# Kernel tuning notes

Hardware: AMD Instinct MI355X
Metric: run time of the kernel (lower is better)

Reference implementation:

```python
import jax, jax.numpy as jnp
import numpy as np

N, E = 50000, 800000
IN, HID, H, OUT = 128, 32, 4, 40
K_SAMPLE, EPS_K = 25.0, 1e-3  # fixed k=25 (no dp_budget), compute_beta eps


def _glorot(key, shape):
    fan_in, fan_out = shape[0], shape[-1]
    lim = jnp.sqrt(6.0 / (fan_in + fan_out))
    return jax.random.uniform(key, shape, jnp.float32, -lim, lim)


def setup_inputs() -> dict:
    key = jax.random.key(0)
    ks = jax.random.split(key, 16)
    x = jax.random.normal(ks[0], (N, IN), jnp.float32)
    edge_index = jax.random.randint(ks[1], (2, E), 0, N, jnp.int64)
    # layer 0: IN -> (H, HID)
    W0 = _glorot(ks[2], (IN, H * HID)); as0 = _glorot(ks[3], (H, HID)); ad0 = _glorot(ks[4], (H, HID)); b0 = jnp.zeros((H * HID,), jnp.float32)
    # layer 1: H*HID -> (H, HID)
    W1 = _glorot(ks[5], (H * HID, H * HID)); as1 = _glorot(ks[6], (H, HID)); ad1 = _glorot(ks[7], (H, HID)); b1 = jnp.zeros((H * HID,), jnp.float32)
    # layer 2: H*HID -> (1, OUT)
    W2 = _glorot(ks[8], (H * HID, OUT)); as2 = _glorot(ks[9], (1, OUT)); ad2 = _glorot(ks[10], (1, OUT)); b2 = jnp.zeros((OUT,), jnp.float32)
    # BatchNorm affine params (batch-stat mode, deterministic)
    g_bn0 = jnp.ones((H * HID,), jnp.float32); be_bn0 = jnp.zeros((H * HID,), jnp.float32)
    g_bn1 = jnp.ones((H * HID,), jnp.float32); be_bn1 = jnp.zeros((H * HID,), jnp.float32)
    return {"x": x, "edge_index": edge_index,
            "W0": W0, "as0": as0, "ad0": ad0, "b0": b0,
            "W1": W1, "as1": as1, "ad1": ad1, "b1": b1,
            "W2": W2, "as2": as2, "ad2": ad2, "b2": b2,
            "g_bn0": g_bn0, "be_bn0": be_bn0, "g_bn1": g_bn1, "be_bn1": be_bn1}


def gat_conv(x, src, dst, W, a_src, a_dst, bias, heads, d_out):
    # PyG GATConv, add_self_loops=False, concat over heads
    h = (x @ W).reshape(-1, heads, d_out)                       # [N,H,D]
    al_s = jnp.sum(h * a_src, axis=-1)                          # [N,H]
    al_d = jnp.sum(h * a_dst, axis=-1)                          # [N,H]
    e = jax.nn.leaky_relu(al_s[src] + al_d[dst], 0.2)           # [E,H]
    m = jax.ops.segment_max(e, dst, num_segments=N)
    m = jnp.where(jnp.isfinite(m), m, 0.0)                      # guard empty segments
    p = jnp.exp(e - m[dst])
    s = jax.ops.segment_sum(p, dst, num_segments=N)
    alpha = p / (s[dst] + 1e-16)                                # segment softmax over incoming edges
    out = jax.ops.segment_sum(alpha[:, :, None] * h[src], dst, num_segments=N)  # [N,H,D]
    return out.reshape(-1, heads * d_out) + bias


def batch_norm(x, gamma, beta):
    mu = jnp.mean(x, axis=0)
    var = jnp.mean(jnp.square(x - mu), axis=0)
    return gamma * (x - mu) * jax.lax.rsqrt(var + 1e-5) + beta


def beta_scale(l):
    return 1.0 + 1.0 / (l + 1.0) * (1.0 / (K_SAMPLE + EPS_K))


def reference(x, edge_index, W0, as0, ad0, b0, W1, as1, ad1, b1, W2, as2, ad2, b2,
              g_bn0, be_bn0, g_bn1, be_bn1):
    src, dst = edge_index[0], edge_index[1]
    h = gat_conv(x, src, dst, W0, as0, ad0, b0, H, HID)
    h = jax.nn.elu(batch_norm(h, g_bn0, be_bn0)) * beta_scale(0)
    h = gat_conv(h, src, dst, W1, as1, ad1, b1, H, HID)
    h = jax.nn.elu(batch_norm(h, g_bn1, be_bn1)) * beta_scale(1)
    h = gat_conv(h, src, dst, W2, as2, ad2, b2, 1, OUT)
    return jax.nn.log_softmax(h, axis=1)
```

## Files before the change

### kernel.cpp

```cpp
#include <hip/hip_runtime.h>
#include <math.h>

#define N_NODES 50000
#define N_EDGES 800000
#define DIN 128
#define DHID 128
#define NH 4
#define HID 32
#define DOUT 40

#define PB 128
#define NPB 391

typedef __fp16 fp16x2 __attribute__((ext_vector_type(2)));

static __device__ __forceinline__ float lrelu(float x) { return x > 0.f ? x : 0.2f * x; }

static __device__ __forceinline__ unsigned int pkh(float a, float b) {
    union { fp16x2 h2; unsigned int u; } cv;
    cv.h2 = __builtin_amdgcn_cvt_pkrtz(a, b);
    return cv.u;
}
static __device__ __forceinline__ unsigned short f2h(float a) {
    union { _Float16 h; unsigned short s; } cv;
    cv.h = (_Float16)a;
    return cv.s;
}

static __device__ __forceinline__ void fma8(float* acc, uint4 w, float p) {
    union { unsigned int u; _Float16 h[2]; } c0, c1, c2, c3;
    c0.u = w.x; c1.u = w.y; c2.u = w.z; c3.u = w.w;
    acc[0] = fmaf((float)c0.h[0], p, acc[0]);
    acc[1] = fmaf((float)c0.h[1], p, acc[1]);
    acc[2] = fmaf((float)c1.h[0], p, acc[2]);
    acc[3] = fmaf((float)c1.h[1], p, acc[3]);
    acc[4] = fmaf((float)c2.h[0], p, acc[4]);
    acc[5] = fmaf((float)c2.h[1], p, acc[5]);
    acc[6] = fmaf((float)c3.h[0], p, acc[6]);
    acc[7] = fmaf((float)c3.h[1], p, acc[7]);
}

static __device__ __forceinline__ float4 bnelu4(float4 x, float4 sc, float4 sh, float bs) {
    float y0 = fmaf(x.x, sc.x, sh.x);
    float y1 = fmaf(x.y, sc.y, sh.y);
    float y2 = fmaf(x.z, sc.z, sh.z);
    float y3 = fmaf(x.w, sc.w, sh.w);
    y0 = (y0 > 0.f ? y0 : __expf(y0) - 1.f) * bs;
    y1 = (y1 > 0.f ? y1 : __expf(y1) - 1.f) * bs;
    y2 = (y2 > 0.f ? y2 : __expf(y2) - 1.f) * bs;
    y3 = (y3 > 0.f ? y3 : __expf(y3) - 1.f) * bs;
    return {y0, y1, y2, y3};
}

__global__ __launch_bounds__(256) void bucket_hist_kernel(const int* __restrict__ dstv, int* __restrict__ bhist) {
    __shared__ int h[PB];
    if (threadIdx.x < PB) h[threadIdx.x] = 0;
    __syncthreads();
    for (int i = blockIdx.x * blockDim.x + threadIdx.x; i < N_EDGES; i += gridDim.x * blockDim.x)
        atomicAdd(&h[(unsigned)dstv[i] / NPB], 1);
    __syncthreads();
    if (threadIdx.x < PB) atomicAdd(&bhist[threadIdx.x], h[threadIdx.x]);
}

__global__ __launch_bounds__(128) void bucket_scan_kernel(const int* __restrict__ bhist,
                                                          int* __restrict__ bucket_base, int* __restrict__ cursor) {
    __shared__ int sA[PB], sB[PB];
    int t = threadIdx.x;
    sA[t] = bhist[t];
    __syncthreads();
    int* s = sA; int* d2 = sB;
    for (int off = 1; off < PB; off <<= 1) {
        d2[t] = s[t] + (t >= off ? s[t - off] : 0);
        __syncthreads();
        int* tmp = s; s = d2; d2 = tmp;
    }
    int excl = s[t] - bhist[t];
    bucket_base[t] = excl;
    cursor[t] = excl;
    if (t == PB - 1) bucket_base[PB] = s[t];
}

__global__ __launch_bounds__(256) void partition_kernel(const int* __restrict__ srcv, const int* __restrict__ dstv,
                                                        int* __restrict__ cursor, unsigned* __restrict__ part) {
    __shared__ unsigned rec[2048];
    __shared__ int cnt[PB], lofs[PB], gbase[PB];
    __shared__ int sA[PB], sB[PB];
    __shared__ int tot_s;
    const int t = threadIdx.x;
    const int base0 = blockIdx.x * 4096;
    for (int round = 0; round < 2; ++round) {
        int rbase = base0 + round * 2048;
        if (t < PB) cnt[t] = 0;
        __syncthreads();
        int myb[8]; int myr[8]; unsigned myrec[8];
#pragma unroll
        for (int i = 0; i < 8; ++i) {
            int e = rbase + i * 256 + t;
            bool valid = e < N_EDGES;
            int sv = valid ? srcv[e] : 0;
            int dv = valid ? dstv[e] : 0;
            myrec[i] = ((unsigned)sv << 16) | (unsigned)dv;
            int b = (unsigned)dv / NPB;
            myb[i] = valid ? b : -1;
            myr[i] = valid ? atomicAdd(&cnt[b], 1) : 0;
        }
        __syncthreads();
        if (t < PB) sA[t] = cnt[t];
        __syncthreads();
        int* s = sA; int* d2 = sB;
        for (int off = 1; off < PB; off <<= 1) {
            if (t < PB) d2[t] = s[t] + (t >= off ? s[t - off] : 0);
            __syncthreads();
            int* tmp = s; s = d2; d2 = tmp;
        }
        if (t < PB) {
            int c = cnt[t];
            lofs[t] = s[t] - c;
            gbase[t] = c > 0 ? atomicAdd(&cursor[t], c) : 0;
            if (t == PB - 1) tot_s = s[t];
        }
        __syncthreads();
#pragma unroll
        for (int i = 0; i < 8; ++i)
            if (myb[i] >= 0) rec[lofs[myb[i]] + myr[i]] = myrec[i];
        __syncthreads();
        int tot = tot_s;
#pragma unroll
        for (int i = 0; i < 8; ++i) {
            int lp = i * 256 + t;
            if (lp < tot) {
                unsigned r = rec[lp];
                int b = (r & 0xFFFFu) / NPB;
                part[gbase[b] + (lp - lofs[b])] = r;
            }
        }
        __syncthreads();
    }
}

__global__ __launch_bounds__(256) void bucket_csr_kernel(const unsigned* __restrict__ part, const int* __restrict__ bucket_base,
                                                         int* __restrict__ row_ptr, int* __restrict__ csr_src) {
    __shared__ int hist[512], sA[512], sB[512], cur[NPB];
    const int b = blockIdx.x, t = threadIdx.x;
    const int base = bucket_base[b];
    const int n = bucket_base[b + 1] - base;
    hist[t] = 0; hist[t + 256] = 0;
    __syncthreads();
    for (int i = t; i < n; i += 256)
        atomicAdd(&hist[(part[base + i] & 0xFFFFu) - b * NPB], 1);
    __syncthreads();
    sA[t] = hist[t]; sA[t + 256] = hist[t + 256];
    __syncthreads();
    int* s = sA; int* d2 = sB;
    for (int off = 1; off < 512; off <<= 1) {
        d2[t] = s[t] + (t >= off ? s[t - off] : 0);
        int u = t + 256;
        d2[u] = s[u] + (u >= off ? s[u - off] : 0);
        __syncthreads();
        int* tmp = s; s = d2; d2 = tmp;
    }
    for (int j = t; j < NPB; j += 256) {
        int node = b * NPB + j;
        int excl = s[j] - hist[j];
        if (node < N_NODES) row_ptr[node] = base + excl;
        cur[j] = excl;
    }
    if (b == PB - 1 && t == 0) row_ptr[N_NODES] = N_EDGES;
    __syncthreads();
    for (int i = t; i < n; i += 256) {
        unsigned r = part[base + i];
        int loc = (int)(r & 0xFFFFu) - b * NPB;
        int p = atomicAdd(&cur[loc], 1);
        csr_src[base + p] = (int)(r >> 16);
    }
}

__global__ __launch_bounds__(256) void gemm128_kernel(
    const float* __restrict__ X, const float* __restrict__ W,
    const float* __restrict__ a_src, const float* __restrict__ a_dst,
    const float* __restrict__ sums, const float* __restrict__ sqs,
    const float* __restrict__ gamma, const float* __restrict__ beta, float bscale, int apply_bn,
    unsigned int* __restrict__ Hout, float* __restrict__ als, float* __restrict__ ald) {
    __shared__ float Xs[32][68];
    __shared__ float Ws[32][64];
    __shared__ float scale_s[DHID], shift_s[DHID];
    const int t = threadIdx.x;
    const int tx = t & 15, ty = t >> 4;
    const int r0 = (blockIdx.x >> 1) * 64;
    const int c0 = (blockIdx.x & 1) * 64;
    const int sr = t >> 2, sa = t & 3;
    const int wk = t >> 4, wc = (t & 15) * 4;

    if (apply_bn && t < DHID) {
        float mu = sums[t] * (1.f / N_NODES);
        float var = sqs[t] * (1.f / N_NODES) - mu * mu;
        float sc = gamma[t] * rsqrtf(var + 1e-5f);
        scale_s[t] = sc;
        shift_s[t] = beta[t] - mu * sc;
    }
    __syncthreads();

    int gr = r0 + sr; gr = gr < N_NODES ? gr : N_NODES - 1;
    const float* Xrow = X + (size_t)gr * 128;
    float4 xpreA = *(const float4*)(Xrow + 8 * sa);
    float4 xpreB = *(const float4*)(Xrow + 8 * sa + 4);
    if (apply_bn) {
        xpreA = bnelu4(xpreA, *(const float4*)(scale_s + 8 * sa), *(const float4*)(shift_s + 8 * sa), bscale);
        xpreB = bnelu4(xpreB, *(const float4*)(scale_s + 8 * sa + 4), *(const float4*)(shift_s + 8 * sa + 4), bscale);
    }
    float4 wpreA = *(const float4*)(W + (size_t)wk * 128 + c0 + wc);
    float4 wpreB = *(const float4*)(W + (size_t)(wk + 16) * 128 + c0 + wc);

    float acc[4][4];
#pragma unroll
    for (int i = 0; i < 4; ++i)
#pragma unroll
        for (int c = 0; c < 4; ++c) acc[i][c] = 0.f;

    for (int step = 0; step < 4; ++step) {
        __syncthreads();
        Xs[8 * sa + 0][sr] = xpreA.x;
        Xs[8 * sa + 1][sr] = xpreA.y;
        Xs[8 * sa + 2][sr] = xpreA.z;
        Xs[8 * sa + 3][sr] = xpreA.w;
        Xs[8 * sa + 4][sr] = xpreB.x;
        Xs[8 * sa + 5][sr] = xpreB.y;
        Xs[8 * sa + 6][sr] = xpreB.z;
        Xs[8 * sa + 7][sr] = xpreB.w;
        *(float4*)&Ws[wk][wc] = wpreA;
        *(float4*)&Ws[wk + 16][wc] = wpreB;
        if (step < 3) {
            int k0 = (step + 1) * 32;
            xpreA = *(const float4*)(Xrow + k0 + 8 * sa);
            xpreB = *(const float4*)(Xrow + k0 + 8 * sa + 4);
            if (apply_bn) {
                xpreA = bnelu4(xpreA, *(const float4*)(scale_s + k0 + 8 * sa), *(const float4*)(shift_s + k0 + 8 * sa), bscale);
                xpreB = bnelu4(xpreB, *(const float4*)(scale_s + k0 + 8 * sa + 4), *(const float4*)(shift_s + k0 + 8 * sa + 4), bscale);
            }
            wpreA = *(const float4*)(W + (size_t)(k0 + wk) * 128 + c0 + wc);
            wpreB = *(const float4*)(W + (size_t)(k0 + wk + 16) * 128 + c0 + wc);
        }
        __syncthreads();
#pragma unroll
        for (int kk = 0; kk < 32; ++kk) {
            float4 xv = *(const float4*)&Xs[kk][4 * ty];
            float4 wv = *(const float4*)&Ws[kk][4 * tx];
            float xr[4] = {xv.x, xv.y, xv.z, xv.w};
            float wr[4] = {wv.x, wv.y, wv.z, wv.w};
#pragma unroll
            for (int i = 0; i < 4; ++i)
#pragma unroll
                for (int c = 0; c < 4; ++c)
                    acc[i][c] = fmaf(xr[i], wr[c], acc[i][c]);
        }
    }
    const int head = (c0 >> 5) + (tx >> 3);
    float asv[4], adv[4];
#pragma unroll
    for (int c = 0; c < 4; ++c) {
        asv[c] = a_src[(head & 1) * 32 + (4 * tx + c) % 32 + (head >> 1) * 64];
        adv[c] = a_dst[(head & 1) * 32 + (4 * tx + c) % 32 + (head >> 1) * 64];
    }
#pragma unroll
    for (int i = 0; i < 4; ++i) {
        int r = r0 + 4 * ty + i;
        bool valid = r < N_NODES;
        if (valid) {
            uint2 pk = {pkh(acc[i][0], acc[i][1]), pkh(acc[i][2], acc[i][3])};
            *(uint2*)(Hout + (size_t)r * 64 + (c0 >> 1) + 2 * tx) = pk;
        }
        float ps = 0.f, pd = 0.f;
#pragma unroll
        for (int c = 0; c < 4; ++c) {
            ps = fmaf(acc[i][c], asv[c], ps);
            pd = fmaf(acc[i][c], adv[c], pd);
        }
#pragma unroll
        for (int off = 1; off < 8; off <<= 1) {
            ps += __shfl_xor(ps, off);
            pd += __shfl_xor(pd, off);
        }
        if (valid && (tx & 7) == 0) {
            als[r * 4 + head] = ps;
            ald[r * 4 + head] = pd;
        }
    }
}

__global__ __launch_bounds__(256) void gemm40_kernel(
    const float* __restrict__ X, const float* __restrict__ W,
    const float* __restrict__ a_src, const float* __restrict__ a_dst,
    const float* __restrict__ sums, const float* __restrict__ sqs,
    const float* __restrict__ gamma, const float* __restrict__ beta, float bscale,
    unsigned short* __restrict__ Hout, float* __restrict__ als, float* __restrict__ ald) {
    __shared__ float Xs[64][36];
    __shared__ float Ws[40][36];
    __shared__ float scale_s[DHID], shift_s[DHID];
    const int t = threadIdx.x;
    const int tx = t & 7, ty = t >> 3;
    const int r0 = blockIdx.x * 64;
    const int sr = t >> 2, sa = t & 3;

    if (t < DHID) {
        float mu = sums[t] * (1.f / N_NODES);
        float var = sqs[t] * (1.f / N_NODES) - mu * mu;
        float sc = gamma[t] * rsqrtf(var + 1e-5f);
        scale_s[t] = sc;
        shift_s[t] = beta[t] - mu * sc;
    }
    __syncthreads();

    int gr = r0 + sr; gr = gr < N_NODES ? gr : N_NODES - 1;
    const float* Xrow = X + (size_t)gr * 128;
    float4 xpreA = bnelu4(*(const float4*)(Xrow + 8 * sa),
                          *(const float4*)(scale_s + 8 * sa), *(const float4*)(shift_s + 8 * sa), bscale);
    float4 xpreB = bnelu4(*(const float4*)(Xrow + 8 * sa + 4),
                          *(const float4*)(scale_s + 8 * sa + 4), *(const float4*)(shift_s + 8 * sa + 4), bscale);
    float wpre[5];
#pragma unroll
    for (int i = 0; i < 5; ++i) wpre[i] = W[t + 256 * i];

    float acc[2][5];
#pragma unroll
    for (int i = 0; i < 2; ++i)
#pragma unroll
        for (int j = 0; j < 5; ++j) acc[i][j] = 0.f;

    for (int step = 0; step < 4; ++step) {
        __syncthreads();
        *(float4*)&Xs[sr][8 * sa] = xpreA;
        *(float4*)&Xs[sr][8 * sa + 4] = xpreB;
#pragma unroll
        for (int i = 0; i < 5; ++i) {
            int idx = t + 256 * i;
            Ws[idx % 40][idx / 40] = wpre[i];
        }
        if (step < 3) {
            int k0 = (step + 1) * 32;
            xpreA = bnelu4(*(const float4*)(Xrow + k0 + 8 * sa),
                           *(const float4*)(scale_s + k0 + 8 * sa), *(const float4*)(shift_s + k0 + 8 * sa), bscale);
            xpreB = bnelu4(*(const float4*)(Xrow + k0 + 8 * sa + 4),
                           *(const float4*)(scale_s + k0 + 8 * sa + 4), *(const float4*)(shift_s + k0 + 8 * sa + 4), bscale);
#pragma unroll
            for (int i = 0; i < 5; ++i) wpre[i] = W[k0 * 40 + t + 256 * i];
        }
        __syncthreads();
#pragma unroll
        for (int kk4 = 0; kk4 < 8; ++kk4) {
            float4 xa = *(const float4*)&Xs[2 * ty][4 * kk4];
            float4 xb = *(const float4*)&Xs[2 * ty + 1][4 * kk4];
#pragma unroll
            for (int j = 0; j < 5; ++j) {
                float4 wv = *(const float4*)&Ws[tx + 8 * j][4 * kk4];
                acc[0][j] = fmaf(xa.x, wv.x, acc[0][j]);
                acc[0][j] = fmaf(xa.y, wv.y, acc[0][j]);
                acc[0][j] = fmaf(xa.z, wv.z, acc[0][j]);
                acc[0][j] = fmaf(xa.w, wv.w, acc[0][j]);
                acc[1][j] = fmaf(xb.x, wv.x, acc[1][j]);
                acc[1][j] = fmaf(xb.y, wv.y, acc[1][j]);
                acc[1][j] = fmaf(xb.z, wv.z, acc[1][j]);
                acc[1][j] = fmaf(xb.w, wv.w, acc[1][j]);
            }
        }
    }
    float asv[5], adv[5];
#pragma unroll
    for (int j = 0; j < 5; ++j) {
        asv[j] = a_src[tx + 8 * j];
        adv[j] = a_dst[tx + 8 * j];
    }
#pragma unroll
    for (int i = 0; i < 2; ++i) {
        int r = r0 + 2 * ty + i;
        bool valid = r < N_NODES;
        if (valid) {
#pragma unroll
            for (int j = 0; j < 5; ++j)
                Hout[(size_t)r * 40 + tx + 8 * j] = f2h(acc[i][j]);
        }
        float ps = 0.f, pd = 0.f;
#pragma unroll
        for (int j = 0; j < 5; ++j) {
            ps = fmaf(acc[i][j], asv[j], ps);
            pd = fmaf(acc[i][j], adv[j], pd);
        }
#pragma unroll
        for (int off = 1; off < 8; off <<= 1) {
            ps += __shfl_xor(ps, off);
            pd += __shfl_xor(pd, off);
        }
        if (valid && tx == 0) {
            als[r] = ps;
            ald[r] = pd;
        }
    }
}

__global__ __launch_bounds__(256) void agg128_kernel(
    const int* __restrict__ row_ptr, const int* __restrict__ csr_src,
    const unsigned int* __restrict__ Ht, const float* __restrict__ als, const float* __restrict__ ald,
    const float* __restrict__ bias, float* __restrict__ out) {
    __shared__ float s_p[4][256];
    __shared__ int s_u[4][64];
    int v = (blockIdx.x * blockDim.x + threadIdx.x) >> 6;
    v = __builtin_amdgcn_readfirstlane(v);
    int lane = threadIdx.x & 63;
    int wslot = threadIdx.x >> 6;
    if (v >= N_NODES) return;
    int beg = row_ptr[v], end = row_ptr[v + 1];
    float4 ad4 = *(const float4*)(ald + (size_t)v * 4);
    const int g = lane >> 4;
    const int li = lane & 15;
    const int hh = li >> 2;
    float tsum = 0.f;
    float acc[8];
#pragma unroll
    for (int j = 0; j < 8; ++j) acc[j] = 0.f;

    for (int cbeg = beg; cbeg < end; cbeg += 64) {
        int cnt = min(64, end - cbeg);
        bool act = lane < cnt;
        int u = act ? csr_src[cbeg + lane] : 0;
        float p0, p1, p2, p3;
        if (act) {
            float4 s4 = *(const float4*)(als + (size_t)u * 4);
            p0 = __expf(lrelu(s4.x + ad4.x));
            p1 = __expf(lrelu(s4.y + ad4.y));
            p2 = __expf(lrelu(s4.z + ad4.z));
            p3 = __expf(lrelu(s4.w + ad4.w));
        } else {
            p0 = p1 = p2 = p3 = 0.f;
        }
        s_u[wslot][lane] = u;
        float4 pv = {p0, p1, p2, p3};
        *(float4*)&s_p[wslot][lane * 4] = pv;
        for (int i = 0; i < cnt; i += 8) {
            int ea = i + g;
            int eb = i + 4 + g;
            int ua = s_u[wslot][ea];
            int ub = s_u[wslot][eb];
            float pa = s_p[wslot][ea * 4 + hh];
            float pb = s_p[wslot][eb * 4 + hh];
            uint4 wa = *(const uint4*)(Ht + (size_t)ua * 64 + li * 4);
            uint4 wb = *(const uint4*)(Ht + (size_t)ub * 64 + li * 4);
            tsum += pa + pb;
            fma8(acc, wa, pa);
            fma8(acc, wb, pb);
        }
    }
#pragma unroll
    for (int j = 0; j < 8; ++j) {
        acc[j] += __shfl_xor(acc[j], 16);
        acc[j] += __shfl_xor(acc[j], 32);
    }
    tsum += __shfl_xor(tsum, 16);
    tsum += __shfl_xor(tsum, 32);
    float inv = 1.f / (tsum + 1e-16f);
    if (g == 0) {
        float4 b0 = *(const float4*)(bias + 8 * li);
        float4 b1 = *(const float4*)(bias + 8 * li + 4);
        float4 o0 = {acc[0] * inv + b0.x, acc[1] * inv + b0.y, acc[2] * inv + b0.z, acc[3] * inv + b0.w};
        float4 o1 = {acc[4] * inv + b1.x, acc[5] * inv + b1.y, acc[6] * inv + b1.z, acc[7] * inv + b1.w};
        *(float4*)(out + (size_t)v * DHID + 8 * li) = o0;
        *(float4*)(out + (size_t)v * DHID + 8 * li + 4) = o1;
    }
}

__global__ __launch_bounds__(256) void agg40_kernel(
    const int* __restrict__ row_ptr, const int* __restrict__ csr_src,
    const uint4* __restrict__ Ht4, const float* __restrict__ als, const float* __restrict__ ald,
    const float* __restrict__ bias, float* __restrict__ out) {
    __shared__ float s_p[4][76];
    __shared__ int s_u[4][76];
    __shared__ float s_red[4][12][41];
    int v = (blockIdx.x * blockDim.x + threadIdx.x) >> 6;
    v = __builtin_amdgcn_readfirstlane(v);
    int lane = threadIdx.x & 63;
    int wslot = threadIdx.x >> 6;
    if (v >= N_NODES) return;
    int beg = row_ptr[v], end = row_ptr[v + 1];
    float adv = ald[v];
    const int g = lane / 5;
    const int li = lane - g * 5;
    const bool gact = lane < 60;
    if (lane < 12) { s_u[wslot][64 + lane] = 0; s_p[wslot][64 + lane] = 0.f; }
    float tsum = 0.f;
    float a[8];
#pragma unroll
    for (int j = 0; j < 8; ++j) a[j] = 0.f;

    for (int cbeg = beg; cbeg < end; cbeg += 64) {
        int cnt = min(64, end - cbeg);
        bool act = lane < cnt;
        int u = act ? csr_src[cbeg + lane] : 0;
        float p = act ? __expf(lrelu(als[u] + adv)) : 0.f;
        s_u[wslot][lane] = u;
        s_p[wslot][lane] = p;
        for (int i = 0; i < cnt; i += 12) {
            int e = i + g;
            int uu = s_u[wslot][e];
            float pp = s_p[wslot][e];
            uint4 w = {0u, 0u, 0u, 0u};
            if (gact) w = Ht4[(size_t)uu * 5 + li];
            if (gact) tsum += pp;
            fma8(a, w, pp);
        }
    }
    if (gact) {
#pragma unroll
        for (int j = 0; j < 8; ++j) s_red[wslot][g][li * 8 + j] = a[j];
        if (li == 0) s_red[wslot][g][40] = tsum;
    }
    bool fown = lane < DOUT;
    float accf = 0.f, T = 0.f;
#pragma unroll
    for (int g2 = 0; g2 < 12; ++g2) {
        if (fown) accf += s_red[wslot][g2][lane];
        T += s_red[wslot][g2][40];
    }
    float inv = 1.f / (T + 1e-16f);
    float z = fown ? (accf * inv + bias[lane]) : -1e30f;
    float zm = z;
#pragma unroll
    for (int off = 1; off < 64; off <<= 1) zm = fmaxf(zm, __shfl_xor(zm, off));
    float se = fown ? __expf(z - zm) : 0.f;
#pragma unroll
    for (int off = 1; off < 64; off <<= 1) se += __shfl_xor(se, off);
    float ls = zm + logf(se);
    if (fown) out[(size_t)v * DOUT + lane] = z - ls;
}

__global__ __launch_bounds__(256) void bn_stats_kernel(const float* __restrict__ X,
                                                       float* __restrict__ sums, float* __restrict__ sqs) {
    const int t = threadIdx.x;
    const int tid = blockIdx.x * 256 + t;
    const float4* X4 = (const float4*)X;
    float4 s = {0.f, 0.f, 0.f, 0.f}, q = {0.f, 0.f, 0.f, 0.f};
    for (int i = tid; i < N_NODES * 32; i += 500 * 256) {
        float4 vv = X4[i];
        s.x += vv.x; s.y += vv.y; s.z += vv.z; s.w += vv.w;
        q.x += vv.x * vv.x; q.y += vv.y * vv.y; q.z += vv.z * vv.z; q.w += vv.w * vv.w;
    }
    __shared__ float ls[1024], lq[1024];
    *(float4*)&ls[t * 4] = s;
    *(float4*)&lq[t * 4] = q;
    __syncthreads();
    if (t < 128) {
        int c4 = t >> 2, j = t & 3;
        float S = 0.f, Q = 0.f;
#pragma unroll
        for (int k = 0; k < 8; ++k) {
            S += ls[(c4 + 32 * k) * 4 + j];
            Q += lq[(c4 + 32 * k) * 4 + j];
        }
        atomicAdd(&sums[t], S);
        atomicAdd(&sqs[t], Q);
    }
}

extern "C" void kernel_launch(void* const* d_in, const int* in_sizes, int n_in,
                              void* d_out, int out_size, void* d_ws, size_t ws_size,
                              hipStream_t stream) {
    (void)in_sizes; (void)n_in; (void)out_size; (void)ws_size;
    const float* x = (const float*)d_in[0];
    const int* ei = (const int*)d_in[1];
    const float* W0 = (const float*)d_in[2];
    const float* as0 = (const float*)d_in[3];
    const float* ad0 = (const float*)d_in[4];
    const float* b0 = (const float*)d_in[5];
    const float* W1 = (const float*)d_in[6];
    const float* as1 = (const float*)d_in[7];
    const float* ad1 = (const float*)d_in[8];
    const float* b1 = (const float*)d_in[9];
    const float* W2 = (const float*)d_in[10];
    const float* as2 = (const float*)d_in[11];
    const float* ad2 = (const float*)d_in[12];
    const float* b2 = (const float*)d_in[13];
    const float* g_bn0 = (const float*)d_in[14];
    const float* be_bn0 = (const float*)d_in[15];
    const float* g_bn1 = (const float*)d_in[16];
    const float* be_bn1 = (const float*)d_in[17];
    float* out = (float*)d_out;

    const int* srcv = ei;
    const int* dstv = ei + N_EDGES;

    char* p = (char*)d_ws;
    auto carve = [&](size_t bytes) {
        char* q = p;
        p += (bytes + 255) & ~(size_t)255;
        return q;
    };
    unsigned int* h_bf = (unsigned int*)carve((size_t)N_NODES * 64 * 4);
    float* agg   = (float*)carve((size_t)N_NODES * DHID * 4);
    float* als   = (float*)carve((size_t)N_NODES * NH * 4);
    float* ald   = (float*)carve((size_t)N_NODES * NH * 4);
    int* row_ptr = (int*)carve((size_t)(N_NODES + 1) * 4);
    int* csr_src = (int*)carve((size_t)N_EDGES * 4);
    unsigned* part = (unsigned*)carve((size_t)N_EDGES * 4);
    int* bhist   = (int*)carve((PB + 512) * 4);
    float* sums0 = (float*)(bhist + PB);
    float* sqs0  = sums0 + 128;
    float* sums1 = sqs0 + 128;
    float* sqs1  = sums1 + 128;
    int* bucket_base = (int*)carve((PB + 1) * 4);
    int* cursor  = (int*)carve(PB * 4);

    const float bs0 = 1.0f + 1.0f / 25.001f;
    const float bs1 = 1.0f + 0.5f / 25.001f;

    const int RT64 = (N_NODES + 63) / 64;
    const int G128B = RT64 * 2;
    const int G40B = RT64;
    const int AB = (N_NODES * 64 + 255) / 256;
    const int PARTB = (N_EDGES + 4095) / 4096;

    hipMemsetAsync(bhist, 0, (PB + 512) * 4, stream);
    bucket_hist_kernel<<<400, 256, 0, stream>>>(dstv, bhist);
    bucket_scan_kernel<<<1, PB, 0, stream>>>(bhist, bucket_base, cursor);
    partition_kernel<<<PARTB, 256, 0, stream>>>(srcv, dstv, cursor, part);
    bucket_csr_kernel<<<PB, 256, 0, stream>>>(part, bucket_base, row_ptr, csr_src);

    gemm128_kernel<<<G128B, 256, 0, stream>>>(x, W0, as0, ad0, nullptr, nullptr, nullptr, nullptr, 1.f, 0, h_bf, als, ald);
    agg128_kernel<<<AB, 256, 0, stream>>>(row_ptr, csr_src, h_bf, als, ald, b0, agg);
    bn_stats_kernel<<<500, 256, 0, stream>>>(agg, sums0, sqs0);

    gemm128_kernel<<<G128B, 256, 0, stream>>>(agg, W1, as1, ad1, sums0, sqs0, g_bn0, be_bn0, bs0, 1, h_bf, als, ald);
    agg128_kernel<<<AB, 256, 0, stream>>>(row_ptr, csr_src, h_bf, als, ald, b1, agg);
    bn_stats_kernel<<<500, 256, 0, stream>>>(agg, sums1, sqs1);

    gemm40_kernel<<<G40B, 256, 0, stream>>>(agg, W2, as2, ad2, sums1, sqs1, g_bn1, be_bn1, bs1, (unsigned short*)h_bf, als, ald);
    agg40_kernel<<<AB, 256, 0, stream>>>(row_ptr, csr_src, (const uint4*)h_bf, als, ald, b2, out);
}
```

Measured before the change: 270.1 us.

## Rewrite 128-wide GEMM with bf16 MFMA and swizzled shared-memory weight fragments

```diff
diff --git a/kernel.cpp b/kernel.cpp
--- a/kernel.cpp
+++ b/kernel.cpp
@@ -13,6 +13,8 @@
 #define NPB 391
 
 typedef __fp16 fp16x2 __attribute__((ext_vector_type(2)));
+using s16x8 = __attribute__((ext_vector_type(8))) short;
+using f32x4v = __attribute__((ext_vector_type(4))) float;
 
 static __device__ __forceinline__ float lrelu(float x) { return x > 0.f ? x : 0.2f * x; }
 
@@ -25,6 +27,11 @@
     union { _Float16 h; unsigned short s; } cv;
     cv.h = (_Float16)a;
     return cv.s;
+}
+static __device__ __forceinline__ unsigned short f2bf(float f) {
+    unsigned int u = __float_as_uint(f);
+    u = (u + 0x7FFFu + ((u >> 16) & 1u)) >> 16;
+    return (unsigned short)u;
 }
 
 static __device__ __forceinline__ void fma8(float* acc, uint4 w, float p) {
@@ -180,16 +187,13 @@
     const float* __restrict__ a_src, const float* __restrict__ a_dst,
     const float* __restrict__ sums, const float* __restrict__ sqs,
     const float* __restrict__ gamma, const float* __restrict__ beta, float bscale, int apply_bn,
-    unsigned int* __restrict__ Hout, float* __restrict__ als, float* __restrict__ ald) {
-    __shared__ float Xs[32][68];
-    __shared__ float Ws[32][64];
+    unsigned short* __restrict__ Hout16, float* __restrict__ als, float* __restrict__ ald) {
+    __shared__ unsigned int Xl[64][68];
+    __shared__ unsigned short Wf[16384];
     __shared__ float scale_s[DHID], shift_s[DHID];
     const int t = threadIdx.x;
-    const int tx = t & 15, ty = t >> 4;
-    const int r0 = (blockIdx.x >> 1) * 64;
-    const int c0 = (blockIdx.x & 1) * 64;
-    const int sr = t >> 2, sa = t & 3;
-    const int wk = t >> 4, wc = (t & 15) * 4;
+    const int w = t >> 6, l = t & 63;
+    const int r0 = blockIdx.x * 64;
 
     if (apply_bn && t < DHID) {
         float mu = sums[t] * (1.f / N_NODES);
@@ -200,89 +204,86 @@
     }
     __syncthreads();
 
-    int gr = r0 + sr; gr = gr < N_NODES ? gr : N_NODES - 1;
-    const float* Xrow = X + (size_t)gr * 128;
-    float4 xpreA = *(const float4*)(Xrow + 8 * sa);
-    float4 xpreB = *(const float4*)(Xrow + 8 * sa + 4);
-    if (apply_bn) {
-        xpreA = bnelu4(xpreA, *(const float4*)(scale_s + 8 * sa), *(const float4*)(shift_s + 8 * sa), bscale);
-        xpreB = bnelu4(xpreB, *(const float4*)(scale_s + 8 * sa + 4), *(const float4*)(shift_s + 8 * sa + 4), bscale);
-    }
-    float4 wpreA = *(const float4*)(W + (size_t)wk * 128 + c0 + wc);
-    float4 wpreB = *(const float4*)(W + (size_t)(wk + 16) * 128 + c0 + wc);
-
-    float acc[4][4];
-#pragma unroll
-    for (int i = 0; i < 4; ++i)
-#pragma unroll
-        for (int c = 0; c < 4; ++c) acc[i][c] = 0.f;
-
-    for (int step = 0; step < 4; ++step) {
-        __syncthreads();
-        Xs[8 * sa + 0][sr] = xpreA.x;
-        Xs[8 * sa + 1][sr] = xpreA.y;
-        Xs[8 * sa + 2][sr] = xpreA.z;
-        Xs[8 * sa + 3][sr] = xpreA.w;
-        Xs[8 * sa + 4][sr] = xpreB.x;
-        Xs[8 * sa + 5][sr] = xpreB.y;
-        Xs[8 * sa + 6][sr] = xpreB.z;
-        Xs[8 * sa + 7][sr] = xpreB.w;
-        *(float4*)&Ws[wk][wc] = wpreA;
-        *(float4*)&Ws[wk + 16][wc] = wpreB;
-        if (step < 3) {
-            int k0 = (step + 1) * 32;
-            xpreA = *(const float4*)(Xrow + k0 + 8 * sa);
-            xpreB = *(const float4*)(Xrow + k0 + 8 * sa + 4);
+    {
+        int sr = t >> 2, sa = t & 3;
+        int gr = r0 + sr; gr = gr < N_NODES ? gr : N_NODES - 1;
+        const float* Xrow = X + (size_t)gr * 128;
+#pragma unroll
+        for (int q = 0; q < 4; ++q) {
+            int k0 = q * 32 + sa * 8;
+            float4 xa = *(const float4*)(Xrow + k0);
+            float4 xb = *(const float4*)(Xrow + k0 + 4);
             if (apply_bn) {
-                xpreA = bnelu4(xpreA, *(const float4*)(scale_s + k0 + 8 * sa), *(const float4*)(shift_s + k0 + 8 * sa), bscale);
-                xpreB = bnelu4(xpreB, *(const float4*)(scale_s + k0 + 8 * sa + 4), *(const float4*)(shift_s + k0 + 8 * sa + 4), bscale);
+                xa = bnelu4(xa, *(const float4*)(scale_s + k0), *(const float4*)(shift_s + k0), bscale);
+                xb = bnelu4(xb, *(const float4*)(scale_s + k0 + 4), *(const float4*)(shift_s + k0 + 4), bscale);
             }
-            wpreA = *(const float4*)(W + (size_t)(k0 + wk) * 128 + c0 + wc);
-            wpreB = *(const float4*)(W + (size_t)(k0 + wk + 16) * 128 + c0 + wc);
-        }
-        __syncthreads();
-#pragma unroll
-        for (int kk = 0; kk < 32; ++kk) {
-            float4 xv = *(const float4*)&Xs[kk][4 * ty];
-            float4 wv = *(const float4*)&Ws[kk][4 * tx];
-            float xr[4] = {xv.x, xv.y, xv.z, xv.w};
-            float wr[4] = {wv.x, wv.y, wv.z, wv.w};
-#pragma unroll
-            for (int i = 0; i < 4; ++i)
-#pragma unroll
-                for (int c = 0; c < 4; ++c)
-                    acc[i][c] = fmaf(xr[i], wr[c], acc[i][c]);
-        }
-    }
-    const int head = (c0 >> 5) + (tx >> 3);
-    float asv[4], adv[4];
-#pragma unroll
-    for (int c = 0; c < 4; ++c) {
-        asv[c] = a_src[(head & 1) * 32 + (4 * tx + c) % 32 + (head >> 1) * 64];
-        adv[c] = a_dst[(head & 1) * 32 + (4 * tx + c) % 32 + (head >> 1) * 64];
-    }
-#pragma unroll
-    for (int i = 0; i < 4; ++i) {
-        int r = r0 + 4 * ty + i;
-        bool valid = r < N_NODES;
+            unsigned int* dst = &Xl[sr][k0 >> 1];
+            dst[0] = (unsigned)f2bf(xa.x) | ((unsigned)f2bf(xa.y) << 16);
+            dst[1] = (unsigned)f2bf(xa.z) | ((unsigned)f2bf(xa.w) << 16);
+            dst[2] = (unsigned)f2bf(xb.x) | ((unsigned)f2bf(xb.y) << 16);
+            dst[3] = (unsigned)f2bf(xb.z) | ((unsigned)f2bf(xb.w) << 16);
+        }
+    }
+#pragma unroll 4
+    for (int i = 0; i < 64; ++i) {
+        int idx = i * 256 + t;
+        int k = idx >> 7, c = idx & 127;
+        float wv = W[idx];
+        int ks = k >> 5, kr = k & 31;
+        int lfrag = ((kr >> 3) << 4) | (c & 15);
+        int slot = lfrag ^ ((lfrag >> 3) & 3);
+        Wf[(((ks << 3) + (c >> 4)) * 64 + slot) * 8 + (kr & 7)] = f2bf(wv);
+    }
+    __syncthreads();
+
+    f32x4v acc[8];
+#pragma unroll
+    for (int ct = 0; ct < 8; ++ct) acc[ct] = {0.f, 0.f, 0.f, 0.f};
+    const int cl = l & 15, g = l >> 4;
+    const int slotR = l ^ ((l >> 3) & 3);
+    const unsigned short* XrowL = (const unsigned short*)&Xl[16 * w + cl][0];
+#pragma unroll
+    for (int ks = 0; ks < 4; ++ks) {
+        s16x8 afrag = *(const s16x8*)(XrowL + ks * 32 + g * 8);
+#pragma unroll
+        for (int ct = 0; ct < 8; ++ct) {
+            s16x8 bfrag = *(const s16x8*)&Wf[(((ks << 3) + ct) * 64 + slotR) * 8];
+            acc[ct] = __builtin_amdgcn_mfma_f32_16x16x32_bf16(afrag, bfrag, acc[ct], 0, 0, 0);
+        }
+    }
+
+    float asv[8], adv[8];
+#pragma unroll
+    for (int ct = 0; ct < 8; ++ct) {
+        asv[ct] = a_src[ct * 16 + cl];
+        adv[ct] = a_dst[ct * 16 + cl];
+    }
+#pragma unroll
+    for (int r = 0; r < 4; ++r) {
+        int node = r0 + 16 * w + 4 * g + r;
+        bool valid = node < N_NODES;
         if (valid) {
-            uint2 pk = {pkh(acc[i][0], acc[i][1]), pkh(acc[i][2], acc[i][3])};
-            *(uint2*)(Hout + (size_t)r * 64 + (c0 >> 1) + 2 * tx) = pk;
-        }
-        float ps = 0.f, pd = 0.f;
-#pragma unroll
-        for (int c = 0; c < 4; ++c) {
-            ps = fmaf(acc[i][c], asv[c], ps);
-            pd = fmaf(acc[i][c], adv[c], pd);
-        }
-#pragma unroll
-        for (int off = 1; off < 8; off <<= 1) {
-            ps += __shfl_xor(ps, off);
-            pd += __shfl_xor(pd, off);
-        }
-        if (valid && (tx & 7) == 0) {
-            als[r * 4 + head] = ps;
-            ald[r * 4 + head] = pd;
+#pragma unroll
+            for (int ct = 0; ct < 8; ++ct)
+                Hout16[(size_t)node * 128 + ct * 16 + cl] = f2h(acc[ct][r]);
+        }
+        float ps[4], pd[4];
+#pragma unroll
+        for (int h = 0; h < 4; ++h) {
+            ps[h] = acc[2 * h][r] * asv[2 * h] + acc[2 * h + 1][r] * asv[2 * h + 1];
+            pd[h] = acc[2 * h][r] * adv[2 * h] + acc[2 * h + 1][r] * adv[2 * h + 1];
+#pragma unroll
+            for (int off = 1; off < 16; off <<= 1) {
+                ps[h] += __shfl_xor(ps[h], off);
+                pd[h] += __shfl_xor(pd[h], off);
+            }
+        }
+        if (valid && cl == 0) {
+#pragma unroll
+            for (int h = 0; h < 4; ++h) {
+                als[node * 4 + h] = ps[h];
+                ald[node * 4 + h] = pd[h];
+            }
         }
     }
 }
@@ -610,7 +611,7 @@
     const float bs1 = 1.0f + 0.5f / 25.001f;
 
     const int RT64 = (N_NODES + 63) / 64;
-    const int G128B = RT64 * 2;
+    const int G128B = RT64;
     const int G40B = RT64;
     const int AB = (N_NODES * 64 + 255) / 256;
     const int PARTB = (N_EDGES + 4095) / 4096;
@@ -621,11 +622,13 @@
     partition_kernel<<<PARTB, 256, 0, stream>>>(srcv, dstv, cursor, part);
     bucket_csr_kernel<<<PB, 256, 0, stream>>>(part, bucket_base, row_ptr, csr_src);
 
-    gemm128_kernel<<<G128B, 256, 0, stream>>>(x, W0, as0, ad0, nullptr, nullptr, nullptr, nullptr, 1.f, 0, h_bf, als, ald);
+    gemm128_kernel<<<G128B, 256, 0, stream>>>(x, W0, as0, ad0, nullptr, nullptr, nullptr, nullptr, 1.f, 0,
+                                              (unsigned short*)h_bf, als, ald);
     agg128_kernel<<<AB, 256, 0, stream>>>(row_ptr, csr_src, h_bf, als, ald, b0, agg);
     bn_stats_kernel<<<500, 256, 0, stream>>>(agg, sums0, sqs0);
 
-    gemm128_kernel<<<G128B, 256, 0, stream>>>(agg, W1, as1, ad1, sums0, sqs0, g_bn0, be_bn0, bs0, 1, h_bf, als, ald);
+    gemm128_kernel<<<G128B, 256, 0, stream>>>(agg, W1, as1, ad1, sums0, sqs0, g_bn0, be_bn0, bs0, 1,
+                                              (unsigned short*)h_bf, als, ald);
     agg128_kernel<<<AB, 256, 0, stream>>>(row_ptr, csr_src, h_bf, als, ald, b1, agg);
     bn_stats_kernel<<<500, 256, 0, stream>>>(agg, sums1, sqs1);
 
```

Result: faster. 248.9 us (-7.9%).
